# Kernel optimization log

Measured on AMD Instinct MI355X. Metric: run time of the kernel, lower is better.

## Reference

```python
import jax, jax.numpy as jnp
import numpy as np

TEMPERATURE = 1.0

def setup_inputs() -> dict:
    key = jax.random.key(0)
    k1, k2 = jax.random.split(key)
    z1 = jax.random.normal(k1, (8, 256, 2048), dtype=jnp.float32)
    z2 = jax.random.normal(k2, (8, 256, 2048), dtype=jnp.float32)
    return {"z1": z1, "z2": z2}

def reference(z1, z2):
    # logits[b, n, m] = sum_s z1[b, s, n] * z2[b, s, m], scaled by temperature
    logits = jnp.einsum('bsn,bsm->bnm', z1, z2) / TEMPERATURE
    # torch F.cross_entropy on (b, C=n, m) with labels[b, m] = m:
    # softmax over axis 1 (n), then gather the diagonal n == m.
    logp = jax.nn.log_softmax(logits, axis=1)        # (b, n, m)
    diag = jnp.diagonal(logp, axis1=1, axis2=2)      # (b, m) = logp[b, m, m]
    return -jnp.mean(diag)
```

## Files before the change

### kernel.cpp

```cpp
#include <hip/hip_runtime.h>
#include <hip/hip_bf16.h>


#define NN 2048
#define SK 256
#define LDST 264
#define LOG2E 1.4426950408889634f
#define LN2   0.6931471805599453f
#define COFF  96.0f

typedef __attribute__((ext_vector_type(8))) short short8;
typedef __attribute__((ext_vector_type(16))) float f32x16;

__device__ __forceinline__ unsigned short f2bf(float f) {
    __hip_bfloat16 h = __float2bfloat16(f);
    unsigned short u; __builtin_memcpy(&u, &h, 2); return u;
}

__device__ __forceinline__ float exp2g(float x) {
#if __has_builtin(__builtin_amdgcn_exp2f)
    return __builtin_amdgcn_exp2f(x);
#else
    return exp2f(x);
#endif
}

__device__ __forceinline__ float log2g(float x) {
#if __has_builtin(__builtin_amdgcn_logf)
    return __builtin_amdgcn_logf(x);
#else
    return log2f(x);
#endif
}

__global__ __launch_bounds__(512) void gemm_lse_kernel(
    const float* __restrict__ z1, const float* __restrict__ z2,
    float* __restrict__ ws_sum, float* __restrict__ ws_diag)
{
    __shared__ unsigned short ldsA[64 * LDST];

    const int bid  = blockIdx.x;
    const int b    = bid & 7;
    const int tile = bid >> 3;
    const int mb   = tile & 7;
    const int ns   = tile >> 3;
    const int tid  = threadIdx.x;
    const int lane = tid & 63;
    const int w    = tid >> 6;
    const int wm   = w >> 1;
    const int wn   = w & 1;
    const int col  = lane & 31;
    const int kg   = lane >> 5;

    const int m0      = mb * 256 + wm * 64;
    const int mcol0   = m0 + col;
    const int mcol1   = m0 + 32 + col;
    const int n_start = ns * 512;

    const float* z1b = z1 + (size_t)b * SK * NN;
    const float* z2b = z2 + (size_t)b * SK * NN;

    short8 bf0[16], bf1[16];
    #pragma unroll
    for (int ks = 0; ks < 16; ++ks) {
        short8 p0, p1;
        #pragma unroll
        for (int j = 0; j < 8; ++j) {
            const int s = ks * 16 + kg * 8 + j;
            p0[j] = (short)f2bf(z2b[s * NN + mcol0] * LOG2E);
            p1[j] = (short)f2bf(z2b[s * NN + mcol1] * LOG2E);
        }
        bf0[ks] = p0; bf1[ks] = p1;
    }

    float apf[4][8];
    auto load_A = [&](int t) {
        const int nbase = n_start + 64 * t;
        #pragma unroll
        for (int r = 0; r < 4; ++r) {
            const int sg = 8 * r + w;
            const float* p = z1b + (size_t)(sg * 8) * NN + nbase + lane;
            #pragma unroll
            for (int j = 0; j < 8; ++j) apf[r][j] = p[(size_t)j * NN];
        }
    };
    auto store_A = [&]() {
        #pragma unroll
        for (int r = 0; r < 4; ++r) {
            const int sg = 8 * r + w;
            short8 pk;
            #pragma unroll
            for (int j = 0; j < 8; ++j) pk[j] = (short)f2bf(apf[r][j]);
            *(short8*)(ldsA + lane * LDST + sg * 8) = pk;
        }
    };

    float srun0 = 0.0f, srun1 = 0.0f;

    load_A(0);
    for (int t = 0; t < 8; ++t) {
        __syncthreads();
        store_A();
        __syncthreads();
        if (t < 7) load_A(t + 1);

        const unsigned short* abase = ldsA + (32 * wn + col) * LDST + kg * 8;

        f32x16 acc0, acc1;
        #pragma unroll
        for (int r = 0; r < 16; ++r) { acc0[r] = -COFF; acc1[r] = -COFF; }

        #pragma unroll
        for (int ks = 0; ks < 16; ++ks) {
            short8 af = *(const short8*)(abase + ks * 16);
            acc0 = __builtin_amdgcn_mfma_f32_32x32x16_bf16(af, bf0[ks], acc0, 0, 0, 0);
            acc1 = __builtin_amdgcn_mfma_f32_32x32x16_bf16(af, bf1[ks], acc1, 0, 0, 0);
        }

        const int nsub = n_start + 64 * t + 32 * wn;
        if (nsub == m0) {
            #pragma unroll
            for (int r = 0; r < 16; ++r) {
                const int row = (r & 3) + 8 * (r >> 2) + 4 * kg;
                if (row == col) ws_diag[b * NN + mcol0] = acc0[r];
            }
        }
        if (nsub == m0 + 32) {
            #pragma unroll
            for (int r = 0; r < 16; ++r) {
                const int row = (r & 3) + 8 * (r >> 2) + 4 * kg;
                if (row == col) ws_diag[b * NN + mcol1] = acc1[r];
            }
        }

        {
            float e0 = 0, e1 = 0, e2 = 0, e3 = 0;
            #pragma unroll
            for (int r = 0; r < 16; r += 4) {
                e0 += exp2g(acc0[r]);     e1 += exp2g(acc0[r + 1]);
                e2 += exp2g(acc0[r + 2]); e3 += exp2g(acc0[r + 3]);
            }
            srun0 += (e0 + e1) + (e2 + e3);
        }
        {
            float e0 = 0, e1 = 0, e2 = 0, e3 = 0;
            #pragma unroll
            for (int r = 0; r < 16; r += 4) {
                e0 += exp2g(acc1[r]);     e1 += exp2g(acc1[r + 1]);
                e2 += exp2g(acc1[r + 2]); e3 += exp2g(acc1[r + 3]);
            }
            srun1 += (e0 + e1) + (e2 + e3);
        }
    }

    srun0 += __shfl_xor(srun0, 32);
    srun1 += __shfl_xor(srun1, 32);
    if (kg == 0) {
        const int slot = ns * 2 + wn;
        ws_sum[(b * 8 + slot) * NN + mcol0] = srun0;
        ws_sum[(b * 8 + slot) * NN + mcol1] = srun1;
    }
}

__global__ __launch_bounds__(256) void merge_kernel(
    const float* __restrict__ ws_sum, const float* __restrict__ ws_diag,
    float* __restrict__ partial)
{
    const int gid = blockIdx.x * 256 + threadIdx.x;
    const int b = gid >> 11, m = gid & (NN - 1);

    float S = 0.0f;
    #pragma unroll
    for (int slot = 0; slot < 8; ++slot)
        S += ws_sum[(b * 8 + slot) * NN + m];
    float c = log2g(S) - ws_diag[gid];

    #pragma unroll
    for (int d = 1; d < 64; d <<= 1) c += __shfl_xor(c, d);
    __shared__ float red[4];
    if ((threadIdx.x & 63) == 0) red[threadIdx.x >> 6] = c;
    __syncthreads();
    if (threadIdx.x == 0)
        partial[blockIdx.x] = red[0] + red[1] + red[2] + red[3];
}

__global__ void final_kernel(const float* __restrict__ partial, float* __restrict__ out)
{
    float v = partial[threadIdx.x];
    #pragma unroll
    for (int d = 1; d < 64; d <<= 1) v += __shfl_xor(v, d);
    if (threadIdx.x == 0) out[0] = v * (LN2 / 16384.0f);
}

extern "C" void kernel_launch(void* const* d_in, const int* in_sizes, int n_in,
                              void* d_out, int out_size, void* d_ws, size_t ws_size,
                              hipStream_t stream)
{
    const float* z1 = (const float*)d_in[0];
    const float* z2 = (const float*)d_in[1];
    float* ws  = (float*)d_ws;
    float* out = (float*)d_out;

    float* ws_sum  = ws;
    float* ws_diag = ws + 131072;
    float* ws_part = ws + 147456;

    gemm_lse_kernel<<<dim3(256), dim3(512), 0, stream>>>(z1, z2, ws_sum, ws_diag);
    merge_kernel<<<dim3(64), dim3(256), 0, stream>>>(ws_sum, ws_diag, ws_part);
    final_kernel<<<dim3(1), dim3(64), 0, stream>>>(ws_part, out);
}
```

Before: 32.38 us.

## Pre-transpose inputs to bf16 and load MFMA fragments directly from global

Adds a transpose kernel that converts z1 and z2 to bf16 in an [n][s] layout, with the log2e scale folded into z2, and writes them to workspace. The GEMM kernel then reads A and B fragments with vectorized contiguous global loads instead of strided fp32 loads, and drops the LDS staging of A. A register rotation prefetches A fragments. This removes uncoalesced strided reads and in-kernel conversion, at the cost of an extra kernel launch and an extra round trip through memory for both inputs.

```diff
diff --git a/kernel.cpp b/kernel.cpp
--- a/kernel.cpp
+++ b/kernel.cpp
@@ -4,7 +4,6 @@
 
 #define NN 2048
 #define SK 256
-#define LDST 264
 #define LOG2E 1.4426950408889634f
 #define LN2   0.6931471805599453f
 #define COFF  96.0f
@@ -33,12 +32,50 @@
 #endif
 }
 
-__global__ __launch_bounds__(512) void gemm_lse_kernel(
+__global__ __launch_bounds__(256) void transpose_kernel(
     const float* __restrict__ z1, const float* __restrict__ z2,
+    unsigned short* __restrict__ z1t, unsigned short* __restrict__ z2t)
+{
+    __shared__ float lds[64][65];
+
+    const int bid  = blockIdx.x;
+    const int arr  = bid >> 10;
+    const int rest = bid & 1023;
+    const int b    = rest >> 7;
+    const int st   = (rest >> 5) & 3;
+    const int nt   = rest & 31;
+
+    const float* in = (arr ? z2 : z1) + (size_t)b * SK * NN + (size_t)(st * 64) * NN + nt * 64;
+    unsigned short* out = (arr ? z2t : z1t) + (size_t)b * NN * SK + (size_t)(nt * 64) * SK + st * 64;
+    const float scale = arr ? LOG2E : 1.0f;
+
+    const int tid = threadIdx.x;
+    const int n4 = tid & 15, sl = tid >> 4;
+    #pragma unroll
+    for (int r = 0; r < 4; ++r) {
+        const int s = r * 16 + sl;
+        float4 v = *(const float4*)(in + (size_t)s * NN + n4 * 4);
+        lds[n4 * 4 + 0][s] = v.x * scale;
+        lds[n4 * 4 + 1][s] = v.y * scale;
+        lds[n4 * 4 + 2][s] = v.z * scale;
+        lds[n4 * 4 + 3][s] = v.w * scale;
+    }
+    __syncthreads();
+
+    const int nr = tid >> 2, q = tid & 3;
+    short8 o0, o1;
+    #pragma unroll
+    for (int i = 0; i < 8; ++i) o0[i] = (short)f2bf(lds[nr][q * 16 + i]);
+    #pragma unroll
+    for (int i = 0; i < 8; ++i) o1[i] = (short)f2bf(lds[nr][q * 16 + 8 + i]);
+    *(short8*)(out + (size_t)nr * SK + q * 16)     = o0;
+    *(short8*)(out + (size_t)nr * SK + q * 16 + 8) = o1;
+}
+
+__global__ __launch_bounds__(512, 2) void gemm_lse_kernel(
+    const unsigned short* __restrict__ z1t, const unsigned short* __restrict__ z2t,
     float* __restrict__ ws_sum, float* __restrict__ ws_diag)
 {
-    __shared__ unsigned short ldsA[64 * LDST];
-
     const int bid  = blockIdx.x;
     const int b    = bid & 7;
     const int tile = bid >> 3;
@@ -52,84 +89,68 @@
     const int col  = lane & 31;
     const int kg   = lane >> 5;
 
-    const int m0      = mb * 256 + wm * 64;
-    const int mcol0   = m0 + col;
-    const int mcol1   = m0 + 32 + col;
-    const int n_start = ns * 512;
-
-    const float* z1b = z1 + (size_t)b * SK * NN;
-    const float* z2b = z2 + (size_t)b * SK * NN;
+    const int m0 = mb * 256 + wm * 64;
+    const int n0 = ns * 512 + wn * 256;
+
+    const unsigned short* z1b = z1t + (size_t)b * NN * SK;
+    const unsigned short* z2b = z2t + (size_t)b * NN * SK;
 
     short8 bf0[16], bf1[16];
-    #pragma unroll
-    for (int ks = 0; ks < 16; ++ks) {
-        short8 p0, p1;
+    {
+        const unsigned short* b0p = z2b + (size_t)(m0 + col) * SK + kg * 8;
+        const unsigned short* b1p = b0p + 32 * SK;
         #pragma unroll
-        for (int j = 0; j < 8; ++j) {
-            const int s = ks * 16 + kg * 8 + j;
-            p0[j] = (short)f2bf(z2b[s * NN + mcol0] * LOG2E);
-            p1[j] = (short)f2bf(z2b[s * NN + mcol1] * LOG2E);
-        }
-        bf0[ks] = p0; bf1[ks] = p1;
-    }
-
-    float apf[4][8];
-    auto load_A = [&](int t) {
-        const int nbase = n_start + 64 * t;
-        #pragma unroll
-        for (int r = 0; r < 4; ++r) {
-            const int sg = 8 * r + w;
-            const float* p = z1b + (size_t)(sg * 8) * NN + nbase + lane;
-            #pragma unroll
-            for (int j = 0; j < 8; ++j) apf[r][j] = p[(size_t)j * NN];
-        }
-    };
-    auto store_A = [&]() {
-        #pragma unroll
-        for (int r = 0; r < 4; ++r) {
-            const int sg = 8 * r + w;
-            short8 pk;
-            #pragma unroll
-            for (int j = 0; j < 8; ++j) pk[j] = (short)f2bf(apf[r][j]);
-            *(short8*)(ldsA + lane * LDST + sg * 8) = pk;
-        }
-    };
-
+        for (int ks = 0; ks < 16; ++ks) {
+            bf0[ks] = *(const short8*)(b0p + ks * 16);
+            bf1[ks] = *(const short8*)(b1p + ks * 16);
+        }
+    }
+
+    const unsigned short* ap = z1b + (size_t)(n0 + col) * SK + kg * 8;
     float srun0 = 0.0f, srun1 = 0.0f;
 
-    load_A(0);
     for (int t = 0; t < 8; ++t) {
-        __syncthreads();
-        store_A();
-        __syncthreads();
-        if (t < 7) load_A(t + 1);
-
-        const unsigned short* abase = ldsA + (32 * wn + col) * LDST + kg * 8;
+        const unsigned short* ab = ap + (size_t)t * 32 * SK;
 
         f32x16 acc0, acc1;
         #pragma unroll
         for (int r = 0; r < 16; ++r) { acc0[r] = -COFF; acc1[r] = -COFF; }
 
+        short8 af0 = *(const short8*)(ab);
+        short8 af1 = *(const short8*)(ab + 16);
+        short8 af2 = *(const short8*)(ab + 32);
+        short8 af3 = *(const short8*)(ab + 48);
         #pragma unroll
         for (int ks = 0; ks < 16; ++ks) {
-            short8 af = *(const short8*)(abase + ks * 16);
-            acc0 = __builtin_amdgcn_mfma_f32_32x32x16_bf16(af, bf0[ks], acc0, 0, 0, 0);
-            acc1 = __builtin_amdgcn_mfma_f32_32x32x16_bf16(af, bf1[ks], acc1, 0, 0, 0);
-        }
-
-        const int nsub = n_start + 64 * t + 32 * wn;
+            short8 cur;
+            if ((ks & 3) == 0) cur = af0;
+            else if ((ks & 3) == 1) cur = af1;
+            else if ((ks & 3) == 2) cur = af2;
+            else cur = af3;
+            if (ks < 12) {
+                short8 nxt = *(const short8*)(ab + (ks + 4) * 16);
+                if ((ks & 3) == 0) af0 = nxt;
+                else if ((ks & 3) == 1) af1 = nxt;
+                else if ((ks & 3) == 2) af2 = nxt;
+                else af3 = nxt;
+            }
+            acc0 = __builtin_amdgcn_mfma_f32_32x32x16_bf16(cur, bf0[ks], acc0, 0, 0, 0);
+            acc1 = __builtin_amdgcn_mfma_f32_32x32x16_bf16(cur, bf1[ks], acc1, 0, 0, 0);
+        }
+
+        const int nsub = n0 + 32 * t;
         if (nsub == m0) {
             #pragma unroll
             for (int r = 0; r < 16; ++r) {
                 const int row = (r & 3) + 8 * (r >> 2) + 4 * kg;
-                if (row == col) ws_diag[b * NN + mcol0] = acc0[r];
+                if (row == col) ws_diag[b * NN + m0 + col] = acc0[r];
             }
         }
         if (nsub == m0 + 32) {
             #pragma unroll
             for (int r = 0; r < 16; ++r) {
                 const int row = (r & 3) + 8 * (r >> 2) + 4 * kg;
-                if (row == col) ws_diag[b * NN + mcol1] = acc1[r];
+                if (row == col) ws_diag[b * NN + m0 + 32 + col] = acc1[r];
             }
         }
 
@@ -151,14 +172,16 @@
             }
             srun1 += (e0 + e1) + (e2 + e3);
         }
+
+        __syncthreads();
     }
 
     srun0 += __shfl_xor(srun0, 32);
     srun1 += __shfl_xor(srun1, 32);
     if (kg == 0) {
         const int slot = ns * 2 + wn;
-        ws_sum[(b * 8 + slot) * NN + mcol0] = srun0;
-        ws_sum[(b * 8 + slot) * NN + mcol1] = srun1;
+        ws_sum[(b * 8 + slot) * NN + m0 + col]      = srun0;
+        ws_sum[(b * 8 + slot) * NN + m0 + 32 + col] = srun1;
     }
 }
 
@@ -198,14 +221,17 @@
 {
     const float* z1 = (const float*)d_in[0];
     const float* z2 = (const float*)d_in[1];
-    float* ws  = (float*)d_ws;
     float* out = (float*)d_out;
 
-    float* ws_sum  = ws;
-    float* ws_diag = ws + 131072;
-    float* ws_part = ws + 147456;
-
-    gemm_lse_kernel<<<dim3(256), dim3(512), 0, stream>>>(z1, z2, ws_sum, ws_diag);
+    char* wsb = (char*)d_ws;
+    unsigned short* z1t = (unsigned short*)wsb;
+    unsigned short* z2t = (unsigned short*)(wsb + (8u << 20));
+    float* ws_sum  = (float*)(wsb + (16u << 20));
+    float* ws_diag = ws_sum + 8 * 8 * NN;
+    float* ws_part = ws_diag + 8 * NN;
+
+    transpose_kernel<<<dim3(2048), dim3(256), 0, stream>>>(z1, z2, z1t, z2t);
+    gemm_lse_kernel<<<dim3(256), dim3(512), 0, stream>>>(z1t, z2t, ws_sum, ws_diag);
     merge_kernel<<<dim3(64), dim3(256), 0, stream>>>(ws_sum, ws_diag, ws_part);
     final_kernel<<<dim3(1), dim3(64), 0, stream>>>(ws_part, out);
 }
```

Result: slower. 58.51 us (+80.7%).
